# Performance work log

Hardware: AMD Instinct MI355X
Metric: run time of the kernel (lower is better)

The kernel has to match this reference:

```python
import jax, jax.numpy as jnp
import numpy as np
from jax import lax

N_NODES = 116
N_EDGES = 1160
D_FEAT = 653  # SAGEConv in/out channels (last dim)


def _sage_max(x, src, dst, w_l, w_r, b):
    # PyG SAGEConv(aggr='max'): out = lin_l(max_j x_j) + lin_r(x)
    # x: [N, C, F]; aggregation over incoming edges per target node.
    msgs = x[src]  # [E, C, F]
    agg = jax.ops.segment_max(msgs, dst, num_segments=N_NODES)
    agg = jnp.where(jnp.isfinite(agg), agg, 0.0)  # empty segments -> 0 (PyG behavior)
    return jnp.einsum('ncf,gf->ncg', agg, w_l) + b + jnp.einsum('ncf,gf->ncg', x, w_r)


def setup_inputs() -> dict:
    key = jax.random.key(0)
    ks = jax.random.split(key, 16)
    inp = {}
    inp['x'] = jax.random.normal(ks[0], (N_NODES, 64, 657), dtype=jnp.float32)
    inp['edge_index'] = jax.random.randint(ks[1], (2, N_EDGES), 0, N_NODES, dtype=jnp.int64)
    # Conv1d(64 -> 256, kernel=5, groups=4): weight [256, 16, 5]
    inp['conv_w'] = jax.random.normal(ks[2], (256, 16, 5), dtype=jnp.float32) * 0.05
    inp['conv_b'] = jax.random.normal(ks[3], (256,), dtype=jnp.float32) * 0.05
    s = 1.0 / np.sqrt(D_FEAT)
    inp['sage_wl'] = jax.random.normal(ks[4], (D_FEAT, D_FEAT), dtype=jnp.float32) * s
    inp['sage_wr'] = jax.random.normal(ks[5], (D_FEAT, D_FEAT), dtype=jnp.float32) * s
    inp['sage_b'] = jnp.zeros((D_FEAT,), dtype=jnp.float32)
    inp['fc1_w'] = jax.random.normal(ks[6], (128, D_FEAT), dtype=jnp.float32) * s
    inp['fc1_b'] = jnp.zeros((128,), dtype=jnp.float32)
    inp['fc2_w'] = jax.random.normal(ks[7], (32, 128), dtype=jnp.float32) * (1.0 / np.sqrt(128))
    inp['fc2_b'] = jnp.zeros((32,), dtype=jnp.float32)
    inp['fc3_w'] = jax.random.normal(ks[8], (4, 32), dtype=jnp.float32) * (1.0 / np.sqrt(32))
    inp['fc3_b'] = jnp.zeros((4,), dtype=jnp.float32)
    return inp


def reference(x, edge_index, conv_w, conv_b, sage_wl, sage_wr, sage_b,
              fc1_w, fc1_b, fc2_w, fc2_b, fc3_w, fc3_b):
    # grouped Conv1d: [N,64,657] -> [N,256,653]
    h = lax.conv_general_dilated(
        x, conv_w, window_strides=(1,), padding='VALID',
        dimension_numbers=('NCH', 'OIH', 'NCH'), feature_group_count=4)
    h = h + conv_b[None, :, None]
    src, dst = edge_index[0], edge_index[1]
    for _ in range(3):  # same SAGEConv layer applied three times
        h = _sage_max(h, src, dst, sage_wl, sage_wr, sage_b)
    # global_mean_pool over the single graph (batch all zeros) then squeeze
    h = h.mean(axis=0)  # [256, 653]
    h = jax.nn.gelu(h @ fc1_w.T + fc1_b, approximate=False)
    h = jax.nn.gelu(h @ fc2_w.T + fc2_b, approximate=False)
    h = h @ fc3_w.T + fc3_b  # [256, 4]
    return jax.nn.softmax(h, axis=1)
```

## Files before the change

kernel.cpp:

```cpp
#include <hip/hip_runtime.h>
#include <hip/hip_bf16.h>
#include <math.h>

#define NN 116
#define NE 1160
#define CCH 256
#define FF 653
#define KP 672
#define MM (NN*CCH)
#define NPAD 768
#define SZH ((size_t)MM*KP)

typedef unsigned short ushort;
typedef short bf16x8 __attribute__((ext_vector_type(8)));
typedef float f32x4 __attribute__((ext_vector_type(4)));

__device__ __forceinline__ float bfbits_to_f(ushort u) {
    unsigned int w = ((unsigned int)u) << 16;
    return __uint_as_float(w);
}
__device__ __forceinline__ ushort f_to_bfbits(float f) {
    unsigned int u = __float_as_uint(f);
    u += 0x7FFFu + ((u >> 16) & 1u);
    return (ushort)(u >> 16);
}

__device__ __forceinline__ void gl_lds16(const void* g, void* l) {
    __builtin_amdgcn_global_load_lds(
        (const __attribute__((address_space(1))) unsigned int*)g,
        (__attribute__((address_space(3))) unsigned int*)l, 16, 0, 0);
}

__global__ void build_csr_k(const int* __restrict__ ei, int* __restrict__ off,
                            int* __restrict__ lst) {
    __shared__ int s_cnt[NN];
    __shared__ int s_off[NN + 1];
    int t = threadIdx.x;
    for (int i = t; i < NN; i += blockDim.x) s_cnt[i] = 0;
    __syncthreads();
    for (int e = t; e < NE; e += blockDim.x) atomicAdd(&s_cnt[ei[NE + e]], 1);
    __syncthreads();
    if (t == 0) {
        s_off[0] = 0;
        for (int i = 0; i < NN; ++i) s_off[i + 1] = s_off[i] + s_cnt[i];
    }
    __syncthreads();
    for (int i = t; i < NN; i += blockDim.x) { off[i] = s_off[i]; s_cnt[i] = 0; }
    if (t == 0) off[NN] = s_off[NN];
    __syncthreads();
    for (int e = t; e < NE; e += blockDim.x) {
        int d = ei[NE + e];
        int p = atomicAdd(&s_cnt[d], 1);
        lst[s_off[d] + p] = ei[e];
    }
}

__global__ void build_wc_k(const float* __restrict__ wl, const float* __restrict__ wr,
                           ushort* __restrict__ wc) {
    int idx = blockIdx.x * 256 + threadIdx.x;
    const int total = 2 * NPAD * KP;
    if (idx >= total) return;
    int k = idx % KP;
    int rem = idx / KP;
    int n = rem % NPAD;
    int p = rem / NPAD;
    float v = 0.f;
    if (n < FF && k < FF) v = (p ? wr : wl)[(size_t)n * FF + k];
    wc[idx] = f_to_bfbits(v);
}

__global__ __launch_bounds__(256) void conv1d_k(
    const float* __restrict__ x, const float* __restrict__ w,
    const float* __restrict__ b, ushort* __restrict__ h) {
    const int f  = blockIdx.x * 256 + threadIdx.x;
    if (f >= KP) return;
    const int n  = blockIdx.y;
    const int o0 = blockIdx.z * 16;
    const int g  = o0 >> 6;
    if (f >= FF) {
#pragma unroll
        for (int oo = 0; oo < 16; ++oo)
            h[(size_t)(n * CCH + o0 + oo) * KP + f] = 0;
        return;
    }
    const float* xp = x + ((size_t)n * 64 + g * 16) * 657 + f;
    const float* wq = w + o0 * 80;
    float acc[16];
#pragma unroll
    for (int oo = 0; oo < 16; ++oo) acc[oo] = b[o0 + oo];
#pragma unroll
    for (int i = 0; i < 16; ++i) {
        float xv[5];
#pragma unroll
        for (int k = 0; k < 5; ++k) xv[k] = xp[i * 657 + k];
#pragma unroll
        for (int oo = 0; oo < 16; ++oo) {
            const float* wp = wq + oo * 80 + i * 5;
            acc[oo] = fmaf(xv[0], wp[0], acc[oo]);
            acc[oo] = fmaf(xv[1], wp[1], acc[oo]);
            acc[oo] = fmaf(xv[2], wp[2], acc[oo]);
            acc[oo] = fmaf(xv[3], wp[3], acc[oo]);
            acc[oo] = fmaf(xv[4], wp[4], acc[oo]);
        }
    }
#pragma unroll
    for (int oo = 0; oo < 16; ++oo)
        h[(size_t)(n * CCH + o0 + oo) * KP + f] = f_to_bfbits(acc[oo]);
}

__global__ void seg_max_k(const ushort* __restrict__ h, ushort* __restrict__ agg,
                          const int* __restrict__ off, const int* __restrict__ lst) {
    int j = blockIdx.x * 256 + threadIdx.x;
    int c = j / 84;
    int chunk = j % 84;
    int n = blockIdx.y;
    int o0 = off[n], o1 = off[n + 1];
    size_t dsti = ((size_t)(n * CCH + c)) * KP + chunk * 8;
    if (o0 == o1) {
        *(uint4*)(agg + dsti) = make_uint4(0, 0, 0, 0);
        return;
    }
    float m[8];
#pragma unroll
    for (int i = 0; i < 8; ++i) m[i] = -3.4e38f;
    for (int e = o0; e < o1; ++e) {
        int s = lst[e];
        const uint4 v = *(const uint4*)(h + ((size_t)(s * CCH + c)) * KP + chunk * 8);
        unsigned int u[4] = {v.x, v.y, v.z, v.w};
#pragma unroll
        for (int q = 0; q < 4; ++q) {
            float lo = __uint_as_float(u[q] << 16);
            float hi = __uint_as_float(u[q] & 0xFFFF0000u);
            m[2*q]   = fmaxf(m[2*q],   lo);
            m[2*q+1] = fmaxf(m[2*q+1], hi);
        }
    }
    unsigned int o[4];
#pragma unroll
    for (int q = 0; q < 4; ++q) {
        unsigned int a = __float_as_uint(m[2*q])   >> 16;
        unsigned int bq = __float_as_uint(m[2*q+1]) & 0xFFFF0000u;
        o[q] = a | bq;
    }
    *(uint4*)(agg + dsti) = make_uint4(o[0], o[1], o[2], o[3]);
}

__global__ __launch_bounds__(256) void sage_gemm_k(
    const ushort* __restrict__ Agg, const ushort* __restrict__ Hcur,
    const ushort* __restrict__ Wc, const float* __restrict__ bias,
    ushort* __restrict__ Hnxt)
{
    __shared__ ushort As[128 * 32];
    __shared__ ushort Bs[128 * 32];
    const int tid  = threadIdx.x;
    const int lane = tid & 63;
    const int wid  = tid >> 6;
    const int bm = blockIdx.x * 128;
    const int bn = blockIdx.y * 128;
    const int wm = (wid >> 1) * 64;
    const int wn = (wid & 1) * 64;

    f32x4 acc[4][4];
#pragma unroll
    for (int i = 0; i < 4; ++i)
#pragma unroll
        for (int j = 0; j < 4; ++j) acc[i][j] = 0.f;

    const int srow   = lane >> 2;
    const int schunk = lane & 3;
    const int schk   = (schunk ^ ((srow >> 1) & 3)) * 8;
    ushort* lA = As + wid * 16 * 32;
    ushort* lB = Bs + wid * 16 * 32;
    const int lr  = lane & 15;
    const int cc  = lane >> 4;
    const int kc  = (cc ^ ((lr >> 1) & 3)) * 8;

    for (int pass = 0; pass < 2; ++pass) {
        const ushort* Ab = pass ? Hcur : Agg;
        const ushort* Wb = Wc + (size_t)pass * NPAD * KP;
        for (int k0 = 0; k0 < KP; k0 += 32) {
            const ushort* ga0 = Ab + (size_t)(bm + wid * 16 + srow) * KP + k0 + schk;
            const ushort* gb0 = Wb + (size_t)(bn + wid * 16 + srow) * KP + k0 + schk;
            gl_lds16(ga0, lA);
            gl_lds16(ga0 + (size_t)64 * KP, lA + 64 * 32);
            gl_lds16(gb0, lB);
            gl_lds16(gb0 + (size_t)64 * KP, lB + 64 * 32);
            __syncthreads();
            bf16x8 af[4], bfr[4];
#pragma unroll
            for (int i = 0; i < 4; ++i)
                af[i] = *(const bf16x8*)&As[(wm + i * 16 + lr) * 32 + kc];
#pragma unroll
            for (int j = 0; j < 4; ++j)
                bfr[j] = *(const bf16x8*)&Bs[(wn + j * 16 + lr) * 32 + kc];
#pragma unroll
            for (int i = 0; i < 4; ++i)
#pragma unroll
                for (int j = 0; j < 4; ++j)
                    acc[i][j] = __builtin_amdgcn_mfma_f32_16x16x32_bf16(
                        af[i], bfr[j], acc[i][j], 0, 0, 0);
            __syncthreads();
        }
    }
    const int lg = lane >> 4;
#pragma unroll
    for (int j = 0; j < 4; ++j) {
        int n = bn + wn + j * 16 + lr;
        if (n >= KP) continue;
        bool valid = n < FF;
        float bv = valid ? bias[n] : 0.f;
#pragma unroll
        for (int i = 0; i < 4; ++i) {
#pragma unroll
            for (int r = 0; r < 4; ++r) {
                int m = bm + wm + i * 16 + lg * 4 + r;
                float v = valid ? (acc[i][j][r] + bv) : 0.f;
                Hnxt[(size_t)m * KP + n] = f_to_bfbits(v);
            }
        }
    }
}

__global__ void pool_k(const ushort* __restrict__ h, float* __restrict__ pool) {
    int j = blockIdx.x * 256 + threadIdx.x;
    if (j >= 256 * 84) return;
    int c = j / 84;
    int chunk = j % 84;
    float s[8];
#pragma unroll
    for (int i = 0; i < 8; ++i) s[i] = 0.f;
    for (int n = 0; n < NN; ++n) {
        const uint4 v = *(const uint4*)(h + ((size_t)(n * CCH + c)) * KP + chunk * 8);
        unsigned int u[4] = {v.x, v.y, v.z, v.w};
#pragma unroll
        for (int q = 0; q < 4; ++q) {
            s[2*q]   += __uint_as_float(u[q] << 16);
            s[2*q+1] += __uint_as_float(u[q] & 0xFFFF0000u);
        }
    }
    const float inv = 1.0f / NN;
    float* dst = pool + (size_t)c * KP + chunk * 8;
#pragma unroll
    for (int i = 0; i < 8; ++i) dst[i] = s[i] * inv;
}

__device__ __forceinline__ float gelu_exact(float v) {
    return 0.5f * v * (1.0f + erff(v * 0.70710678118654752f));
}

__global__ void head_k(const float* __restrict__ pool,
                       const float* __restrict__ w1, const float* __restrict__ b1,
                       const float* __restrict__ w2, const float* __restrict__ b2,
                       const float* __restrict__ w3, const float* __restrict__ b3,
                       float* __restrict__ out) {
    __shared__ float row[FF];
    __shared__ float h1[128];
    __shared__ float h2[32];
    __shared__ float sc[4];
    const int c = blockIdx.x;
    const int t = threadIdx.x;
    for (int i = t; i < FF; i += 128) row[i] = pool[(size_t)c * KP + i];
    __syncthreads();
    {
        const float* wp = w1 + (size_t)t * FF;
        float s = b1[t];
        for (int i = 0; i < FF; ++i) s = fmaf(row[i], wp[i], s);
        h1[t] = gelu_exact(s);
    }
    __syncthreads();
    if (t < 32) {
        const float* wp = w2 + (size_t)t * 128;
        float s = b2[t];
#pragma unroll
        for (int i = 0; i < 128; ++i) s = fmaf(h1[i], wp[i], s);
        h2[t] = gelu_exact(s);
    }
    __syncthreads();
    if (t < 4) {
        const float* wp = w3 + (size_t)t * 32;
        float s = b3[t];
#pragma unroll
        for (int i = 0; i < 32; ++i) s = fmaf(h2[i], wp[i], s);
        sc[t] = s;
    }
    __syncthreads();
    if (t < 4) {
        float mx = fmaxf(fmaxf(sc[0], sc[1]), fmaxf(sc[2], sc[3]));
        float e0 = __expf(sc[0] - mx), e1 = __expf(sc[1] - mx);
        float e2 = __expf(sc[2] - mx), e3 = __expf(sc[3] - mx);
        float inv = 1.0f / (e0 + e1 + e2 + e3);
        float ev = (t == 0) ? e0 : (t == 1) ? e1 : (t == 2) ? e2 : e3;
        out[(size_t)c * 4 + t] = ev * inv;
    }
}

extern "C" void kernel_launch(void* const* d_in, const int* in_sizes, int n_in,
                              void* d_out, int out_size, void* d_ws, size_t ws_size,
                              hipStream_t stream) {
    const float* x      = (const float*)d_in[0];
    const int*   ei     = (const int*)  d_in[1];
    const float* conv_w = (const float*)d_in[2];
    const float* conv_b = (const float*)d_in[3];
    const float* wl     = (const float*)d_in[4];
    const float* wr     = (const float*)d_in[5];
    const float* sb     = (const float*)d_in[6];
    const float* fc1w   = (const float*)d_in[7];
    const float* fc1b   = (const float*)d_in[8];
    const float* fc2w   = (const float*)d_in[9];
    const float* fc2b   = (const float*)d_in[10];
    const float* fc3w   = (const float*)d_in[11];
    const float* fc3b   = (const float*)d_in[12];
    float* out = (float*)d_out;

    ushort* hA  = (ushort*)d_ws;
    ushort* hB  = hA + SZH;
    ushort* agg = hB + SZH;
    ushort* wc  = agg + SZH;
    float*  pool = (float*)(wc + (size_t)2 * NPAD * KP);
    int*    off  = (int*)(pool + (size_t)CCH * KP);
    int*    lst  = off + 128;

    build_csr_k<<<1, 256, 0, stream>>>(ei, off, lst);
    build_wc_k<<<(2 * NPAD * KP + 255) / 256, 256, 0, stream>>>(wl, wr, wc);
    {
        dim3 cgrid(3, NN, 16);
        conv1d_k<<<cgrid, 256, 0, stream>>>(x, conv_w, conv_b, hA);
    }

    dim3 sg_grid(84, NN);
    dim3 gm_grid(MM / 128, NPAD / 128);
    ushort* cur = hA;
    ushort* nxt = hB;
    for (int layer = 0; layer < 3; ++layer) {
        seg_max_k<<<sg_grid, 256, 0, stream>>>(cur, agg, off, lst);
        sage_gemm_k<<<gm_grid, 256, 0, stream>>>(agg, cur, wc, sb, nxt);
        ushort* tmp = cur; cur = nxt; nxt = tmp;
    }
    pool_k<<<84, 256, 0, stream>>>(cur, pool);
    head_k<<<CCH, 128, 0, stream>>>(pool, fc1w, fc1b, fc2w, fc2b, fc3w, fc3b, out);
}
```

Baseline: 641.8 us.

## Commute mean-pool through final linear SAGE layer and remap GEMM tiles per XCD

```diff
diff --git a/kernel.cpp b/kernel.cpp
--- a/kernel.cpp
+++ b/kernel.cpp
@@ -9,6 +9,7 @@
 #define KP 672
 #define MM (NN*CCH)
 #define NPAD 768
+#define NT6 (NPAD/128)
 #define SZH ((size_t)MM*KP)
 
 typedef unsigned short ushort;
@@ -145,6 +146,78 @@
     *(uint4*)(agg + dsti) = make_uint4(o[0], o[1], o[2], o[3]);
 }
 
+__global__ void seg_pool_k(const ushort* __restrict__ h, float* __restrict__ part,
+                           const int* __restrict__ off, const int* __restrict__ lst) {
+    int j = blockIdx.x * 256 + threadIdx.x;
+    int c = j / 84;
+    int chunk = j % 84;
+    int nq = blockIdx.y;
+    float s[8];
+#pragma unroll
+    for (int i = 0; i < 8; ++i) s[i] = 0.f;
+    for (int n = nq * 29; n < nq * 29 + 29; ++n) {
+        int o0 = off[n], o1 = off[n + 1];
+        if (o0 == o1) continue;
+        float m[8];
+#pragma unroll
+        for (int i = 0; i < 8; ++i) m[i] = -3.4e38f;
+        for (int e = o0; e < o1; ++e) {
+            int sr = lst[e];
+            const uint4 v = *(const uint4*)(h + ((size_t)(sr * CCH + c)) * KP + chunk * 8);
+            unsigned int u[4] = {v.x, v.y, v.z, v.w};
+#pragma unroll
+            for (int q = 0; q < 4; ++q) {
+                float lo = __uint_as_float(u[q] << 16);
+                float hi = __uint_as_float(u[q] & 0xFFFF0000u);
+                m[2*q]   = fmaxf(m[2*q],   lo);
+                m[2*q+1] = fmaxf(m[2*q+1], hi);
+            }
+        }
+#pragma unroll
+        for (int i = 0; i < 8; ++i) s[i] += m[i];
+    }
+    float* dst = part + ((size_t)(nq * CCH + c)) * KP + chunk * 8;
+#pragma unroll
+    for (int i = 0; i < 8; ++i) dst[i] = s[i];
+}
+
+__global__ void combine_k(const float* __restrict__ part, ushort* __restrict__ aggP) {
+    int j = blockIdx.x * 256 + threadIdx.x;
+    int c = j / 84;
+    int chunk = j % 84;
+    const float inv = 1.0f / NN;
+#pragma unroll 1
+    for (int i = 0; i < 8; ++i) {
+        size_t o = ((size_t)c) * KP + chunk * 8 + i;
+        float s = part[o] + part[(size_t)CCH * KP + o]
+                + part[(size_t)2 * CCH * KP + o] + part[(size_t)3 * CCH * KP + o];
+        aggP[o] = f_to_bfbits(s * inv);
+    }
+}
+
+__global__ void pool_k(const ushort* __restrict__ h, ushort* __restrict__ poolm) {
+    int j = blockIdx.x * 256 + threadIdx.x;
+    if (j >= 256 * 84) return;
+    int c = j / 84;
+    int chunk = j % 84;
+    float s[8];
+#pragma unroll
+    for (int i = 0; i < 8; ++i) s[i] = 0.f;
+    for (int n = 0; n < NN; ++n) {
+        const uint4 v = *(const uint4*)(h + ((size_t)(n * CCH + c)) * KP + chunk * 8);
+        unsigned int u[4] = {v.x, v.y, v.z, v.w};
+#pragma unroll
+        for (int q = 0; q < 4; ++q) {
+            s[2*q]   += __uint_as_float(u[q] << 16);
+            s[2*q+1] += __uint_as_float(u[q] & 0xFFFF0000u);
+        }
+    }
+    const float inv = 1.0f / NN;
+    ushort* dst = poolm + (size_t)c * KP + chunk * 8;
+#pragma unroll
+    for (int i = 0; i < 8; ++i) dst[i] = f_to_bfbits(s[i] * inv);
+}
+
 __global__ __launch_bounds__(256) void sage_gemm_k(
     const ushort* __restrict__ Agg, const ushort* __restrict__ Hcur,
     const ushort* __restrict__ Wc, const float* __restrict__ bias,
@@ -152,11 +225,18 @@
 {
     __shared__ ushort As[128 * 32];
     __shared__ ushort Bs[128 * 32];
+    const int bid = blockIdx.x;
+    const int nwg = gridDim.x;
+    const int q   = nwg >> 3, r = nwg & 7;
+    const int xcd = bid & 7,  jj = bid >> 3;
+    const int wgid = (xcd < r ? xcd * (q + 1) : r * (q + 1) + (xcd - r) * q) + jj;
+    const int mt = wgid / NT6;
+    const int nt = wgid - mt * NT6;
+    const int bm = mt * 128;
+    const int bn = nt * 128;
     const int tid  = threadIdx.x;
     const int lane = tid & 63;
     const int wid  = tid >> 6;
-    const int bm = blockIdx.x * 128;
-    const int bn = blockIdx.y * 128;
     const int wm = (wid >> 1) * 64;
     const int wn = (wid & 1) * 64;
 
@@ -212,43 +292,20 @@
 #pragma unroll
         for (int i = 0; i < 4; ++i) {
 #pragma unroll
-            for (int r = 0; r < 4; ++r) {
-                int m = bm + wm + i * 16 + lg * 4 + r;
-                float v = valid ? (acc[i][j][r] + bv) : 0.f;
+            for (int rgi = 0; rgi < 4; ++rgi) {
+                int m = bm + wm + i * 16 + lg * 4 + rgi;
+                float v = valid ? (acc[i][j][rgi] + bv) : 0.f;
                 Hnxt[(size_t)m * KP + n] = f_to_bfbits(v);
             }
         }
     }
 }
 
-__global__ void pool_k(const ushort* __restrict__ h, float* __restrict__ pool) {
-    int j = blockIdx.x * 256 + threadIdx.x;
-    if (j >= 256 * 84) return;
-    int c = j / 84;
-    int chunk = j % 84;
-    float s[8];
-#pragma unroll
-    for (int i = 0; i < 8; ++i) s[i] = 0.f;
-    for (int n = 0; n < NN; ++n) {
-        const uint4 v = *(const uint4*)(h + ((size_t)(n * CCH + c)) * KP + chunk * 8);
-        unsigned int u[4] = {v.x, v.y, v.z, v.w};
-#pragma unroll
-        for (int q = 0; q < 4; ++q) {
-            s[2*q]   += __uint_as_float(u[q] << 16);
-            s[2*q+1] += __uint_as_float(u[q] & 0xFFFF0000u);
-        }
-    }
-    const float inv = 1.0f / NN;
-    float* dst = pool + (size_t)c * KP + chunk * 8;
-#pragma unroll
-    for (int i = 0; i < 8; ++i) dst[i] = s[i] * inv;
-}
-
 __device__ __forceinline__ float gelu_exact(float v) {
     return 0.5f * v * (1.0f + erff(v * 0.70710678118654752f));
 }
 
-__global__ void head_k(const float* __restrict__ pool,
+__global__ void head_k(const ushort* __restrict__ pool,
                        const float* __restrict__ w1, const float* __restrict__ b1,
                        const float* __restrict__ w2, const float* __restrict__ b2,
                        const float* __restrict__ w3, const float* __restrict__ b3,
@@ -259,7 +316,7 @@
     __shared__ float sc[4];
     const int c = blockIdx.x;
     const int t = threadIdx.x;
-    for (int i = t; i < FF; i += 128) row[i] = pool[(size_t)c * KP + i];
+    for (int i = t; i < FF; i += 128) row[i] = bfbits_to_f(pool[(size_t)c * KP + i]);
     __syncthreads();
     {
         const float* wp = w1 + (size_t)t * FF;
@@ -312,12 +369,15 @@
     const float* fc3b   = (const float*)d_in[12];
     float* out = (float*)d_out;
 
-    ushort* hA  = (ushort*)d_ws;
-    ushort* hB  = hA + SZH;
-    ushort* agg = hB + SZH;
-    ushort* wc  = agg + SZH;
-    float*  pool = (float*)(wc + (size_t)2 * NPAD * KP);
-    int*    off  = (int*)(pool + (size_t)CCH * KP);
+    ushort* hA   = (ushort*)d_ws;
+    ushort* hB   = hA + SZH;
+    ushort* agg  = hB + SZH;
+    ushort* wc   = agg + SZH;
+    ushort* aggP = wc + (size_t)2 * NPAD * KP;
+    ushort* h2P  = aggP + (size_t)CCH * KP;
+    ushort* poolt= h2P + (size_t)CCH * KP;
+    float*  part = (float*)(poolt + (size_t)CCH * KP);
+    int*    off  = (int*)(part + (size_t)4 * CCH * KP);
     int*    lst  = off + 128;
 
     build_csr_k<<<1, 256, 0, stream>>>(ei, off, lst);
@@ -328,14 +388,13 @@
     }
 
     dim3 sg_grid(84, NN);
-    dim3 gm_grid(MM / 128, NPAD / 128);
-    ushort* cur = hA;
-    ushort* nxt = hB;
-    for (int layer = 0; layer < 3; ++layer) {
-        seg_max_k<<<sg_grid, 256, 0, stream>>>(cur, agg, off, lst);
-        sage_gemm_k<<<gm_grid, 256, 0, stream>>>(agg, cur, wc, sb, nxt);
-        ushort* tmp = cur; cur = nxt; nxt = tmp;
-    }
-    pool_k<<<84, 256, 0, stream>>>(cur, pool);
-    head_k<<<CCH, 128, 0, stream>>>(pool, fc1w, fc1b, fc2w, fc2b, fc3w, fc3b, out);
-}
+    seg_max_k<<<sg_grid, 256, 0, stream>>>(hA, agg, off, lst);
+    sage_gemm_k<<<MM / 128 * NT6, 256, 0, stream>>>(agg, hA, wc, sb, hB);
+    seg_max_k<<<sg_grid, 256, 0, stream>>>(hB, agg, off, lst);
+    sage_gemm_k<<<MM / 128 * NT6, 256, 0, stream>>>(agg, hB, wc, sb, hA);
+    seg_pool_k<<<dim3(84, 4), 256, 0, stream>>>(hA, part, off, lst);
+    combine_k<<<84, 256, 0, stream>>>(part, aggP);
+    pool_k<<<84, 256, 0, stream>>>(hA, h2P);
+    sage_gemm_k<<<(CCH / 128) * NT6, 256, 0, stream>>>(aggP, h2P, wc, sb, poolt);
+    head_k<<<CCH, 128, 0, stream>>>(poolt, fc1w, fc1b, fc2w, fc2b, fc3w, fc3b, out);
+}
```

Measured after the change: 656.0 us. 2.2% more time.
